# Kernel optimization log

Hardware: AMD Instinct MI355X
Metric: run time of the kernel (lower is better)

The kernel has to match this reference:

```python
import jax, jax.numpy as jnp
import numpy as np

K = 1024          # num_embeddings
D = 128           # embedding_dim
COMMITMENT_COST = 0.25


def setup_inputs() -> dict:
    key = jax.random.key(0)
    k1, k2 = jax.random.split(key)
    inputs = jax.random.normal(k1, (16, D, 4096), dtype=jnp.float32)
    codebook = jax.random.normal(k2, (K, D), dtype=jnp.float32)
    return {"inputs": inputs, "codebook": codebook}


def reference(inputs, codebook):
    # inputs: [B, D, T]; codebook: [K, D]
    B, Dd, T = inputs.shape
    flat = jnp.transpose(inputs, (0, 2, 1)).reshape(-1, Dd)  # [N, D], N = B*T
    N = flat.shape[0]

    d = (jnp.sum(flat * flat, axis=1, keepdims=True)
         + jnp.sum(codebook * codebook, axis=1)
         - 2.0 * flat @ codebook.T)
    idx = jnp.argmin(d, axis=1)  # [N]

    # gather-based quantization (same math as one-hot @ codebook)
    quantized = codebook[idx]                                   # [N, D]
    quantized = quantized.reshape(B, T, Dd).transpose(0, 2, 1)  # [B, D, T]

    # commitment loss (quantized detached; stop_gradient irrelevant in fwd)
    e_latent_loss = jnp.mean((jax.lax.stop_gradient(quantized) - inputs) ** 2)
    loss = COMMITMENT_COST * e_latent_loss

    # straight-through estimator
    quantized_st = inputs + jax.lax.stop_gradient(quantized - inputs)

    # perplexity from code usage histogram (= mean of one-hot encodings)
    counts = jnp.zeros((codebook.shape[0],), dtype=jnp.float32).at[idx].add(1.0)
    avg_probs = counts / N
    perplexity = jnp.exp(-jnp.sum(avg_probs * jnp.log(avg_probs + 1e-10)))

    return loss, quantized_st, perplexity, idx.reshape(B, T)
```

## Files before the change

### kernel.cpp

```cpp
#include <hip/hip_runtime.h>

#define T_FULL 4096
#define D 128
#define K 1024
#define NVEC 65536
#define BDT 8388608
#define BT 128
#define NBLK (NVEC / BT)
#define KT 64
#define NIT (K / KT)
#define PLANE_B (K * D * 2)
#define TILE_B (2 * KT * D * 2)

typedef _Float16 f16x8 __attribute__((ext_vector_type(8)));
typedef float f32x4 __attribute__((ext_vector_type(4)));

#define MFMA(a, b, c) __builtin_amdgcn_mfma_f32_16x16x32_f16((a), (b), (c), 0, 0, 0)

#define GLOAD_LDS(g, l)                                                        \
  __builtin_amdgcn_global_load_lds(                                            \
      (const __attribute__((address_space(1))) unsigned int*)(g),              \
      (__attribute__((address_space(3))) unsigned int*)(l), 16, 0, 0)

__global__ __launch_bounds__(128) void prep_kernel(const float* __restrict__ cb,
    float* __restrict__ ee, _Float16* __restrict__ E1, _Float16* __restrict__ E2,
    unsigned int* __restrict__ counts, unsigned int* __restrict__ done,
    float* __restrict__ loss_acc) {
  int k = blockIdx.x, d = threadIdx.x;
  if (d == 0) {
    counts[k] = 0u;
    if (k == 0) { *done = 0u; *loss_acc = 0.f; }
  }
  float e = cb[k * D + d];
  float v = e * e;
#pragma unroll
  for (int o = 32; o > 0; o >>= 1) v += __shfl_down(v, o, 64);
  __shared__ float tmp[2];
  if ((d & 63) == 0) tmp[d >> 6] = v;
  __syncthreads();
  if (d == 0) ee[k] = tmp[0] + tmp[1];

  float s = 2.0f * e;
  _Float16 h1 = (_Float16)s;
  _Float16 h2 = (_Float16)(s - (float)h1);
  E1[k * D + d] = h1;
  E2[k * D + d] = h2;
}

__global__ __launch_bounds__(256, 2) void vq_main(
    const float* __restrict__ inp, const float* __restrict__ cb,
    const float* __restrict__ ee, const _Float16* __restrict__ Eplanes,
    unsigned int* __restrict__ counts, unsigned int* __restrict__ done,
    float* __restrict__ loss_acc, float* __restrict__ out) {
  __shared__ __align__(16) _Float16 Bs[2 * 2 * KT * D];
  __shared__ float ee_sh[K];
  __shared__ int   midx[BT];
  __shared__ float lred[4];
  __shared__ int   lastf;

  float* out_q   = out + 1;
  float* out_idx = out + 2 + BDT;

  const int tid  = threadIdx.x;
  const int lane = tid & 63;
  const int w    = tid >> 6;
  const int c    = lane & 15;
  const int q    = lane >> 4;
  const int b    = blockIdx.x >> 5;
  const int t0   = (blockIdx.x & 31) * BT;

  unsigned soff[8], slds[8];
#pragma unroll
  for (int i = 0; i < 8; ++i) {
    int flat = tid + i * 256;
    int p    = flat >> 10;
    int s    = flat & 1023;
    int code = s >> 4;
    int dgp  = s & 15;
    int dg   = dgp ^ (code & 15);
    soff[i] = (unsigned)(p * PLANE_B + code * 256 + dg * 16);
    slds[i] = (unsigned)(flat * 16);
  }
  const char* Eb = (const char*)Eplanes;

#pragma unroll
  for (int i = 0; i < 8; ++i)
    GLOAD_LDS(Eb + soff[i], (char*)Bs + slds[i]);

  f16x8 A1[2][4], A2[2][4];
  {
    const float* xin = inp + (size_t)b * D * T_FULL + t0 + w * 32 + c;
#pragma unroll
    for (int n = 0; n < 2; ++n)
#pragma unroll
      for (int dc = 0; dc < 4; ++dc) {
        f16x8 a1, a2;
#pragma unroll
        for (int j = 0; j < 8; ++j) {
          int d = dc * 32 + q * 8 + j;
          float x = xin[(size_t)d * T_FULL + n * 16];
          _Float16 h1 = (_Float16)x;
          _Float16 h2 = (_Float16)(x - (float)h1);
          a1[j] = h1; a2[j] = h2;
        }
        A1[n][dc] = a1; A2[n][dc] = a2;
      }
  }
#pragma unroll
  for (int i = tid; i < K; i += 256) ee_sh[i] = ee[i];
  __syncthreads();

  float bv[2][4];
  int   bi[2][4];
#pragma unroll
  for (int n = 0; n < 2; ++n)
#pragma unroll
    for (int r = 0; r < 4; ++r) { bv[n][r] = 3.4e38f; bi[n][r] = 0; }

  for (int it = 0; it < NIT; ++it) {
    const int kt = it * KT;
    const int bb = it & 1;

    if (it) __syncthreads();

    if (it != NIT - 1) {
      const int ktn = kt + KT;
      const unsigned lbo = (unsigned)((bb ^ 1) * TILE_B);
#pragma unroll
      for (int i = 0; i < 8; ++i)
        GLOAD_LDS(Eb + (size_t)ktn * 256 + soff[i], (char*)Bs + lbo + slds[i]);
    }

    f32x4 acc[2][4];
#pragma unroll
    for (int n = 0; n < 2; ++n)
#pragma unroll
      for (int kf = 0; kf < 4; ++kf) acc[n][kf] = (f32x4){0.f, 0.f, 0.f, 0.f};

    const char* Bp = (const char*)Bs + bb * TILE_B;
#pragma unroll
    for (int dc = 0; dc < 4; ++dc) {
      const int sw = ((dc * 4 + q) ^ c) * 16;
      f16x8 B1[4], B2[4];
#pragma unroll
      for (int kf = 0; kf < 4; ++kf) {
        const int ro = (kf * 16 + c) * 256 + sw;
        B1[kf] = *(const f16x8*)(Bp + ro);
        B2[kf] = *(const f16x8*)(Bp + 16384 + ro);
      }
#pragma unroll
      for (int n = 0; n < 2; ++n)
#pragma unroll
        for (int kf = 0; kf < 4; ++kf) {
          f32x4 a = acc[n][kf];
          a = MFMA(A1[n][dc], B1[kf], a);
          a = MFMA(A1[n][dc], B2[kf], a);
          a = MFMA(A2[n][dc], B1[kf], a);
          acc[n][kf] = a;
        }
    }

#pragma unroll
    for (int kf = 0; kf < 4; ++kf) {
      const int code = kt + kf * 16 + c;
      const float eev = ee_sh[code];
#pragma unroll
      for (int n = 0; n < 2; ++n)
#pragma unroll
        for (int r = 0; r < 4; ++r) {
          float dist = eev - acc[n][kf][r];
          if (dist < bv[n][r]) { bv[n][r] = dist; bi[n][r] = code; }
        }
    }
  }

#pragma unroll
  for (int m = 1; m <= 8; m <<= 1)
#pragma unroll
    for (int n = 0; n < 2; ++n)
#pragma unroll
      for (int r = 0; r < 4; ++r) {
        float ov = __shfl_xor(bv[n][r], m, 64);
        int   oi = __shfl_xor(bi[n][r], m, 64);
        if (ov < bv[n][r] || (ov == bv[n][r] && oi < bi[n][r])) {
          bv[n][r] = ov; bi[n][r] = oi;
        }
      }
  if (c == 0) {
#pragma unroll
    for (int n = 0; n < 2; ++n)
#pragma unroll
      for (int r = 0; r < 4; ++r)
        midx[w * 32 + n * 16 + q * 4 + r] = bi[n][r];
  }
  __syncthreads();

  if (tid < BT) {
    int ki = midx[tid];
    out_idx[(size_t)b * T_FULL + t0 + tid] = (float)ki;
    atomicAdd(&counts[ki], 1u);
  }

  float lsum = 0.f;
  {
    const int t  = tid & 127;
    const int dh = tid >> 7;
    const int kq = midx[t];
    const float* crow = cb + (size_t)kq * D + dh * 64;
    const float* xrow = inp + ((size_t)b * D + dh * 64) * T_FULL + t0 + t;
    float*       qrow = out_q + ((size_t)b * D + dh * 64) * T_FULL + t0 + t;
#pragma unroll
    for (int dd = 0; dd < 64; dd += 4) {
      float4 qv = *(const float4*)(crow + dd);
      float x0 = xrow[(size_t)(dd + 0) * T_FULL];
      float x1 = xrow[(size_t)(dd + 1) * T_FULL];
      float x2 = xrow[(size_t)(dd + 2) * T_FULL];
      float x3 = xrow[(size_t)(dd + 3) * T_FULL];
      float df;
      df = qv.x - x0; lsum = fmaf(df, df, lsum); qrow[(size_t)(dd + 0) * T_FULL] = qv.x;
      df = qv.y - x1; lsum = fmaf(df, df, lsum); qrow[(size_t)(dd + 1) * T_FULL] = qv.y;
      df = qv.z - x2; lsum = fmaf(df, df, lsum); qrow[(size_t)(dd + 2) * T_FULL] = qv.z;
      df = qv.w - x3; lsum = fmaf(df, df, lsum); qrow[(size_t)(dd + 3) * T_FULL] = qv.w;
    }
  }
#pragma unroll
  for (int o = 32; o > 0; o >>= 1) lsum += __shfl_down(lsum, o, 64);
  if (lane == 0) lred[w] = lsum;
  __syncthreads();
  if (tid == 0) {
    atomicAdd(loss_acc, lred[0] + lred[1] + lred[2] + lred[3]);
    __threadfence();
    unsigned ticket = atomicAdd(done, 1u);
    lastf = (ticket == NBLK - 1) ? 1 : 0;
  }
  __syncthreads();

  if (lastf) {
    __threadfence();
    float ent = 0.f;
#pragma unroll
    for (int i = tid; i < K; i += 256) {
      float cnt = (float)atomicAdd(&counts[i], 0u);
      float p = cnt * (1.0f / (float)NVEC);
      ent = fmaf(p, logf(p + 1e-10f), ent);
    }
#pragma unroll
    for (int o = 32; o > 0; o >>= 1) ent += __shfl_down(ent, o, 64);
    if (lane == 0) lred[w] = ent;
    __syncthreads();
    if (tid == 0) {
      float e = lred[0] + lred[1] + lred[2] + lred[3];
      float l = atomicAdd(loss_acc, 0.f);
      out[0]       = 0.25f * (l / (float)BDT);
      out[1 + BDT] = expf(-e);
    }
  }
}

extern "C" void kernel_launch(void* const* d_in, const int* in_sizes, int n_in,
                              void* d_out, int out_size, void* d_ws, size_t ws_size,
                              hipStream_t stream) {
  const float* inp = (const float*)d_in[0];
  const float* cb  = (const float*)d_in[1];
  float* out = (float*)d_out;

  char* ws = (char*)d_ws;
  unsigned int* counts  = (unsigned int*)ws;
  unsigned int* done    = (unsigned int*)(ws + 4096);
  float*        lossacc = (float*)(ws + 4160);
  float*        ee      = (float*)(ws + 8192);
  _Float16*     E1      = (_Float16*)(ws + 12288);
  _Float16*     E2      = (_Float16*)(ws + 12288 + PLANE_B);

  prep_kernel<<<K, 128, 0, stream>>>(cb, ee, E1, E2, counts, done, lossacc);
  vq_main<<<NBLK, 256, 0, stream>>>(inp, cb, ee, E1, counts, done, lossacc, out);
}
```

Baseline: 184.6 us.

## Load codebook fragments directly into registers, dropping LDS staging and block barriers

```diff
diff --git a/kernel.cpp b/kernel.cpp
--- a/kernel.cpp
+++ b/kernel.cpp
@@ -7,20 +7,15 @@
 #define BDT 8388608
 #define BT 128
 #define NBLK (NVEC / BT)
-#define KT 64
-#define NIT (K / KT)
+#define KG 16
+#define NG (K / KG)
 #define PLANE_B (K * D * 2)
-#define TILE_B (2 * KT * D * 2)
+#define GSTRIDE (KG * 256)
 
 typedef _Float16 f16x8 __attribute__((ext_vector_type(8)));
 typedef float f32x4 __attribute__((ext_vector_type(4)));
 
 #define MFMA(a, b, c) __builtin_amdgcn_mfma_f32_16x16x32_f16((a), (b), (c), 0, 0, 0)
-
-#define GLOAD_LDS(g, l)                                                        \
-  __builtin_amdgcn_global_load_lds(                                            \
-      (const __attribute__((address_space(1))) unsigned int*)(g),              \
-      (__attribute__((address_space(3))) unsigned int*)(l), 16, 0, 0)
 
 __global__ __launch_bounds__(128) void prep_kernel(const float* __restrict__ cb,
     float* __restrict__ ee, _Float16* __restrict__ E1, _Float16* __restrict__ E2,
@@ -47,12 +42,13 @@
   E2[k * D + d] = h2;
 }
 
-__global__ __launch_bounds__(256, 2) void vq_main(
+__global__ __launch_bounds__(256)
+__attribute__((amdgpu_waves_per_eu(2, 2)))
+void vq_main(
     const float* __restrict__ inp, const float* __restrict__ cb,
     const float* __restrict__ ee, const _Float16* __restrict__ Eplanes,
     unsigned int* __restrict__ counts, unsigned int* __restrict__ done,
     float* __restrict__ loss_acc, float* __restrict__ out) {
-  __shared__ __align__(16) _Float16 Bs[2 * 2 * KT * D];
   __shared__ float ee_sh[K];
   __shared__ int   midx[BT];
   __shared__ float lred[4];
@@ -69,23 +65,8 @@
   const int b    = blockIdx.x >> 5;
   const int t0   = (blockIdx.x & 31) * BT;
 
-  unsigned soff[8], slds[8];
-#pragma unroll
-  for (int i = 0; i < 8; ++i) {
-    int flat = tid + i * 256;
-    int p    = flat >> 10;
-    int s    = flat & 1023;
-    int code = s >> 4;
-    int dgp  = s & 15;
-    int dg   = dgp ^ (code & 15);
-    soff[i] = (unsigned)(p * PLANE_B + code * 256 + dg * 16);
-    slds[i] = (unsigned)(flat * 16);
-  }
-  const char* Eb = (const char*)Eplanes;
-
-#pragma unroll
-  for (int i = 0; i < 8; ++i)
-    GLOAD_LDS(Eb + soff[i], (char*)Bs + slds[i]);
+  const char* E1p = (const char*)Eplanes + c * 256 + q * 16;
+  const char* E2p = E1p + PLANE_B;
 
   f16x8 A1[2][4], A2[2][4];
   {
@@ -117,62 +98,57 @@
 #pragma unroll
     for (int r = 0; r < 4; ++r) { bv[n][r] = 3.4e38f; bi[n][r] = 0; }
 
-  for (int it = 0; it < NIT; ++it) {
-    const int kt = it * KT;
-    const int bb = it & 1;
-
-    if (it) __syncthreads();
-
-    if (it != NIT - 1) {
-      const int ktn = kt + KT;
-      const unsigned lbo = (unsigned)((bb ^ 1) * TILE_B);
-#pragma unroll
-      for (int i = 0; i < 8; ++i)
-        GLOAD_LDS(Eb + (size_t)ktn * 256 + soff[i], (char*)Bs + lbo + slds[i]);
-    }
-
-    f32x4 acc[2][4];
-#pragma unroll
-    for (int n = 0; n < 2; ++n)
-#pragma unroll
-      for (int kf = 0; kf < 4; ++kf) acc[n][kf] = (f32x4){0.f, 0.f, 0.f, 0.f};
-
-    const char* Bp = (const char*)Bs + bb * TILE_B;
-#pragma unroll
-    for (int dc = 0; dc < 4; ++dc) {
-      const int sw = ((dc * 4 + q) ^ c) * 16;
-      f16x8 B1[4], B2[4];
-#pragma unroll
-      for (int kf = 0; kf < 4; ++kf) {
-        const int ro = (kf * 16 + c) * 256 + sw;
-        B1[kf] = *(const f16x8*)(Bp + ro);
-        B2[kf] = *(const f16x8*)(Bp + 16384 + ro);
-      }
-#pragma unroll
-      for (int n = 0; n < 2; ++n)
-#pragma unroll
-        for (int kf = 0; kf < 4; ++kf) {
-          f32x4 a = acc[n][kf];
-          a = MFMA(A1[n][dc], B1[kf], a);
-          a = MFMA(A1[n][dc], B2[kf], a);
-          a = MFMA(A2[n][dc], B1[kf], a);
-          acc[n][kf] = a;
-        }
-    }
-
-#pragma unroll
-    for (int kf = 0; kf < 4; ++kf) {
-      const int code = kt + kf * 16 + c;
-      const float eev = ee_sh[code];
-#pragma unroll
-      for (int n = 0; n < 2; ++n)
-#pragma unroll
-        for (int r = 0; r < 4; ++r) {
-          float dist = eev - acc[n][kf][r];
-          if (dist < bv[n][r]) { bv[n][r] = dist; bi[n][r] = code; }
-        }
-    }
-  }
+  f16x8 B1a[4], B2a[4], B1b[4], B2b[4];
+
+#define LOADG(S, g)                                                            \
+  do {                                                                         \
+    const char* _p1 = E1p + (size_t)(g) * GSTRIDE;                             \
+    const char* _p2 = E2p + (size_t)(g) * GSTRIDE;                             \
+    _Pragma("unroll")                                                          \
+    for (int dc = 0; dc < 4; ++dc) {                                           \
+      B1##S[dc] = *(const f16x8*)(_p1 + dc * 64);                              \
+      B2##S[dc] = *(const f16x8*)(_p2 + dc * 64);                              \
+    }                                                                          \
+  } while (0)
+
+#define COMPG(S, g)                                                            \
+  do {                                                                         \
+    f32x4 accM[2], accC[2];                                                    \
+    accM[0] = (f32x4){0.f, 0.f, 0.f, 0.f};                                     \
+    accM[1] = (f32x4){0.f, 0.f, 0.f, 0.f};                                     \
+    accC[0] = (f32x4){0.f, 0.f, 0.f, 0.f};                                     \
+    accC[1] = (f32x4){0.f, 0.f, 0.f, 0.f};                                     \
+    _Pragma("unroll")                                                          \
+    for (int dc = 0; dc < 4; ++dc) {                                           \
+      _Pragma("unroll")                                                        \
+      for (int n = 0; n < 2; ++n) {                                            \
+        accM[n] = MFMA(A1[n][dc], B1##S[dc], accM[n]);      \
+        f32x4 t_ = accC[n];                                                    \
+        t_ = MFMA(A1[n][dc], B2##S[dc], t_);                                   \
+        t_ = MFMA(A2[n][dc], B1##S[dc], t_);                                   \
+        accC[n] = t_;                                                          \
+      }                                                                        \
+    }                                                                          \
+    const int   code = (g) * KG + c;                                           \
+    const float eev  = ee_sh[code];                                            \
+    _Pragma("unroll")                                                          \
+    for (int n = 0; n < 2; ++n)                                                \
+      _Pragma("unroll")                                                        \
+      for (int r = 0; r < 4; ++r) {                                            \
+        float dist = eev - accM[n][r] - accC[n][r];                            \
+        if (dist < bv[n][r]) { bv[n][r] = dist; bi[n][r] = code; }             \
+      }                                                                        \
+  } while (0)
+
+  LOADG(a, 0);
+  for (int gg = 0; gg < NG / 2; ++gg) {
+    LOADG(b, 2 * gg + 1);
+    COMPG(a, 2 * gg);
+    if (gg < NG / 2 - 1) LOADG(a, 2 * gg + 2);
+    COMPG(b, 2 * gg + 1);
+  }
+#undef LOADG
+#undef COMPG
 
 #pragma unroll
   for (int m = 1; m <= 8; m <<= 1)
```

Measured after the change: 260.5 us. 1.41x slower.

## Split fused VQ kernel into separate GEMM-argmin and epilogue kernels

Applied to the files above, without the earlier changes.

```diff
diff --git a/kernel.cpp b/kernel.cpp
--- a/kernel.cpp
+++ b/kernel.cpp
@@ -11,6 +11,8 @@
 #define NIT (K / KT)
 #define PLANE_B (K * D * 2)
 #define TILE_B (2 * KT * D * 2)
+#define EBT 64
+#define NEB (NVEC / EBT)
 
 typedef _Float16 f16x8 __attribute__((ext_vector_type(8)));
 typedef float f32x4 __attribute__((ext_vector_type(4)));
@@ -47,19 +49,11 @@
   E2[k * D + d] = h2;
 }
 
-__global__ __launch_bounds__(256, 2) void vq_main(
-    const float* __restrict__ inp, const float* __restrict__ cb,
-    const float* __restrict__ ee, const _Float16* __restrict__ Eplanes,
-    unsigned int* __restrict__ counts, unsigned int* __restrict__ done,
-    float* __restrict__ loss_acc, float* __restrict__ out) {
+__global__ __launch_bounds__(256, 2) void vq_gemm(
+    const float* __restrict__ inp, const float* __restrict__ ee,
+    const _Float16* __restrict__ Eplanes, int* __restrict__ wsm) {
   __shared__ __align__(16) _Float16 Bs[2 * 2 * KT * D];
   __shared__ float ee_sh[K];
-  __shared__ int   midx[BT];
-  __shared__ float lred[4];
-  __shared__ int   lastf;
-
-  float* out_q   = out + 1;
-  float* out_idx = out + 2 + BDT;
 
   const int tid  = threadIdx.x;
   const int lane = tid & 63;
@@ -187,30 +181,52 @@
         }
       }
   if (c == 0) {
+    int* wm = wsm + (size_t)b * T_FULL + t0;
 #pragma unroll
     for (int n = 0; n < 2; ++n)
 #pragma unroll
       for (int r = 0; r < 4; ++r)
-        midx[w * 32 + n * 16 + q * 4 + r] = bi[n][r];
-  }
-  __syncthreads();
-
-  if (tid < BT) {
-    int ki = midx[tid];
+        wm[w * 32 + n * 16 + q * 4 + r] = bi[n][r];
+  }
+}
+
+__global__ __launch_bounds__(256) void vq_epi(
+    const float* __restrict__ inp, const float* __restrict__ cb,
+    const int* __restrict__ wsm,
+    unsigned int* __restrict__ counts, unsigned int* __restrict__ done,
+    float* __restrict__ loss_acc, float* __restrict__ out) {
+  __shared__ int   midx[EBT];
+  __shared__ float lred[4];
+  __shared__ int   lastf;
+
+  float* out_q   = out + 1;
+  float* out_idx = out + 2 + BDT;
+
+  const int tid  = threadIdx.x;
+  const int lane = tid & 63;
+  const int w    = tid >> 6;
+  const int tb   = blockIdx.x;
+  const int b    = tb >> 6;
+  const int t0   = (tb & 63) * EBT;
+
+  if (tid < EBT) {
+    int ki = wsm[(size_t)b * T_FULL + t0 + tid];
+    midx[tid] = ki;
     out_idx[(size_t)b * T_FULL + t0 + tid] = (float)ki;
     atomicAdd(&counts[ki], 1u);
   }
+  __syncthreads();
 
   float lsum = 0.f;
   {
-    const int t  = tid & 127;
-    const int dh = tid >> 7;
+    const int t  = tid & 63;
+    const int dq = tid >> 6;
     const int kq = midx[t];
-    const float* crow = cb + (size_t)kq * D + dh * 64;
-    const float* xrow = inp + ((size_t)b * D + dh * 64) * T_FULL + t0 + t;
-    float*       qrow = out_q + ((size_t)b * D + dh * 64) * T_FULL + t0 + t;
-#pragma unroll
-    for (int dd = 0; dd < 64; dd += 4) {
+    const float* crow = cb + (size_t)kq * D + dq * 32;
+    const float* xrow = inp + ((size_t)b * D + dq * 32) * T_FULL + t0 + t;
+    float*       qrow = out_q + ((size_t)b * D + dq * 32) * T_FULL + t0 + t;
+#pragma unroll
+    for (int dd = 0; dd < 32; dd += 4) {
       float4 qv = *(const float4*)(crow + dd);
       float x0 = xrow[(size_t)(dd + 0) * T_FULL];
       float x1 = xrow[(size_t)(dd + 1) * T_FULL];
@@ -231,7 +247,7 @@
     atomicAdd(loss_acc, lred[0] + lred[1] + lred[2] + lred[3]);
     __threadfence();
     unsigned ticket = atomicAdd(done, 1u);
-    lastf = (ticket == NBLK - 1) ? 1 : 0;
+    lastf = (ticket == NEB - 1) ? 1 : 0;
   }
   __syncthreads();
 
@@ -271,7 +287,9 @@
   float*        ee      = (float*)(ws + 8192);
   _Float16*     E1      = (_Float16*)(ws + 12288);
   _Float16*     E2      = (_Float16*)(ws + 12288 + PLANE_B);
+  int*          wsm     = (int*)(ws + 12288 + 2 * PLANE_B);
 
   prep_kernel<<<K, 128, 0, stream>>>(cb, ee, E1, E2, counts, done, lossacc);
-  vq_main<<<NBLK, 256, 0, stream>>>(inp, cb, ee, E1, counts, done, lossacc, out);
-}
+  vq_gemm<<<NBLK, 256, 0, stream>>>(inp, ee, E1, wsm);
+  vq_epi<<<NEB, 256, 0, stream>>>(inp, cb, wsm, counts, done, lossacc, out);
+}
```

Result: slower. 211.0 us (+14.3%).
